# Kernel tuning notes

Measured on AMD Instinct MI355X. Metric: run time of the kernel, lower is better.

The kernel has to match this reference:

```python
import jax, jax.numpy as jnp
import numpy as np

K = 2
NOISE_STD = 1.0

def setup_inputs() -> dict:
    key = jax.random.key(0)
    k1, k2, k3 = jax.random.split(key, 3)
    N, D, E = 131072, 1024, 64
    x = jax.random.normal(k1, (N, D), dtype=jnp.float32)
    W = jax.random.normal(k2, (E, D), dtype=jnp.float32) * (1.0 / np.sqrt(D))
    b = jnp.zeros((E,), dtype=jnp.float32)
    noise = jax.random.normal(k3, (N, E), dtype=jnp.float32)
    return {"x": x, "W": W, "b": b, "noise": noise}

def reference(x, W, b, noise) -> jnp.ndarray:
    # clean logits: [N, E]
    clean_logits = jnp.einsum('nd,ed->ne', x, W) + b
    noisy_logits = clean_logits + noise * NOISE_STD
    topk_vals, topk_idx = jax.lax.top_k(noisy_logits, K)  # [N, K]
    topk_softmax = jax.nn.softmax(topk_vals, axis=-1)     # [N, K]
    rows = jnp.arange(x.shape[0])[:, None]                 # [N, 1]
    gate_weights = jnp.zeros_like(clean_logits).at[rows, topk_idx].set(topk_softmax)
    return gate_weights
```

## Files before the change

kernel.cpp:

```cpp
#include <hip/hip_runtime.h>
#include <math.h>


#define NEXP   64
#define BLOCK  256
#define TILE_M 128
#define DFIX   1024
#define KCF    32
#define NCH    32
#define NBUF   3
#define XCHB   16384
#define WCHB   8192
#define TAU    1e-3f
#define CAP    4096
#define WS_W_OFF 32768

typedef __attribute__((ext_vector_type(8)))  short bf16x8;
typedef __attribute__((ext_vector_type(16))) float f32x16;

__device__ __forceinline__ bool beats(float v, int e, float vo, int eo) {
    return (v > vo) || (v == vo && e < eo);
}

__device__ __forceinline__ void split2(float f0, float f1, unsigned int& hi, unsigned int& lo) {
    unsigned int u0 = __float_as_uint(f0), u1 = __float_as_uint(f1);
    unsigned int h0 = u0 & 0xFFFF0000u,  h1 = u1 & 0xFFFF0000u;
    float l0 = f0 - __uint_as_float(h0);
    float l1 = f1 - __uint_as_float(h1);
    hi = (u0 >> 16) | h1;
    lo = (__float_as_uint(l0) >> 16) | (__float_as_uint(l1) & 0xFFFF0000u);
}

__device__ __forceinline__ void gl_lds16(const void* g, void* l) {
    __builtin_amdgcn_global_load_lds((const __attribute__((address_space(1))) void*)g,
                                     (__attribute__((address_space(3))) void*)l,
                                     16, 0, 0);
}

__global__ void convW_kernel(const float* __restrict__ W, char* __restrict__ wsW) {
    const int e = blockIdx.x;
    const int t = threadIdx.x;
    const float* wp = W + e * DFIX + t * 8;
    float4 a  = *(const float4*)wp;
    float4 bq = *(const float4*)(wp + 4);
    unsigned int h[4], l[4];
    split2(a.x,  a.y,  h[0], l[0]);
    split2(a.z,  a.w,  h[1], l[1]);
    split2(bq.x, bq.y, h[2], l[2]);
    split2(bq.z, bq.w, h[3], l[3]);
    const int kk   = t >> 1;
    const int lh   = t & 1;
    const int lane = lh * 32 + (e & 31);
    const int g    = e >> 5;
    char* base = wsW + (size_t)(kk * 4 + g * 2) * 1024 + lane * 16;
    *(uint4*)(base)        = make_uint4(h[0], h[1], h[2], h[3]);
    *(uint4*)(base + 1024) = make_uint4(l[0], l[1], l[2], l[3]);
}

__global__ __launch_bounds__(BLOCK, 2)
void gate_mfma(const float* __restrict__ x, const float* __restrict__ bvec,
               const float* __restrict__ noise, const char* __restrict__ wsW,
               float* __restrict__ out, unsigned int* __restrict__ flags) {
    __shared__ __align__(16) char lds[NBUF * (XCHB + WCHB)];
    char* xls = lds;
    char* wls = lds + NBUF * XCHB;

    const int tid  = threadIdx.x;
    const int wv   = tid >> 6;
    const int lane = tid & 63;
    const int e0   = lane & 31;
    const int lh   = lane >> 5;
    const int blkRow0 = blockIdx.x * TILE_M;
    const int rowBase = blkRow0 + wv * 32;
    const int lr      = wv * 32 + e0;
    const int phase   = blockIdx.x & 31;

    f32x16 acc0 = (f32x16)0.0f;
    f32x16 acc1 = (f32x16)0.0f;

    auto STAGE = [&](int gc, int sl) {
        char* xb = xls + sl * XCHB;
        char* wb = wls + sl * WCHB;
        const size_t kbyte = (size_t)gc * (KCF * 4);
        #pragma unroll
        for (int j = 0; j < 4; j++) {
            const int s   = wv * 256 + j * 64 + lane;
            const int row = s >> 3;
            const int sp  = s & 7;
            const int seg = sp ^ (row & 7);
            const char* gp = (const char*)(x + (size_t)(blkRow0 + row) * DFIX)
                             + kbyte + seg * 16;
            gl_lds16(gp, xb + (size_t)(wv * 256 + j * 64) * 16);
        }
        #pragma unroll
        for (int i = 0; i < 2; i++) {
            const int fl = wv * 2 + i;
            const char* gp = wsW + (size_t)gc * WCHB + fl * 1024 + lane * 16;
            gl_lds16(gp, wb + fl * 1024);
        }
    };

    auto COMPUTE = [&](int sl) {
        const char* xb = xls + sl * XCHB;
        const char* wb = wls + sl * WCHB;
        #pragma unroll
        for (int ks = 0; ks < 2; ks++) {
            const int t0 = ks * 4 + lh * 2;
            const int4 xq0 = *(const int4*)(xb + lr * 128 + ((t0    ) ^ (lr & 7)) * 16);
            const int4 xq1 = *(const int4*)(xb + lr * 128 + ((t0 + 1) ^ (lr & 7)) * 16);
            const float4 xa = *(const float4*)&xq0;
            const float4 xc = *(const float4*)&xq1;
            union { bf16x8 v; unsigned int u[4]; } ah, al;
            split2(xa.x, xa.y, ah.u[0], al.u[0]);
            split2(xa.z, xa.w, ah.u[1], al.u[1]);
            split2(xc.x, xc.y, ah.u[2], al.u[2]);
            split2(xc.z, xc.w, ah.u[3], al.u[3]);
            union { bf16x8 v; int4 q; } b0h, b0l, b1h, b1l;
            b0h.q = *(const int4*)(wb + (ks * 4 + 0) * 1024 + lane * 16);
            b0l.q = *(const int4*)(wb + (ks * 4 + 1) * 1024 + lane * 16);
            b1h.q = *(const int4*)(wb + (ks * 4 + 2) * 1024 + lane * 16);
            b1l.q = *(const int4*)(wb + (ks * 4 + 3) * 1024 + lane * 16);
            acc0 = __builtin_amdgcn_mfma_f32_32x32x16_bf16(ah.v, b0h.v, acc0, 0, 0, 0);
            acc1 = __builtin_amdgcn_mfma_f32_32x32x16_bf16(ah.v, b1h.v, acc1, 0, 0, 0);
            acc0 = __builtin_amdgcn_mfma_f32_32x32x16_bf16(ah.v, b0l.v, acc0, 0, 0, 0);
            acc1 = __builtin_amdgcn_mfma_f32_32x32x16_bf16(ah.v, b1l.v, acc1, 0, 0, 0);
            acc0 = __builtin_amdgcn_mfma_f32_32x32x16_bf16(al.v, b0h.v, acc0, 0, 0, 0);
            acc1 = __builtin_amdgcn_mfma_f32_32x32x16_bf16(al.v, b1h.v, acc1, 0, 0, 0);
        }
    };

    STAGE(phase, 0);
    int slc = 0;
    #pragma unroll 1
    for (int c = 0; c < NCH - 1; c++) {
        const int sln = (slc + 1 == NBUF) ? 0 : slc + 1;
        STAGE((c + 1 + phase) & (NCH - 1), sln);
        asm volatile("s_waitcnt vmcnt(6)" ::: "memory");
        __builtin_amdgcn_s_barrier();
        __builtin_amdgcn_sched_barrier(0);
        COMPUTE(slc);
        slc = sln;
    }
    asm volatile("s_waitcnt vmcnt(0)" ::: "memory");
    __builtin_amdgcn_s_barrier();
    __builtin_amdgcn_sched_barrier(0);
    COMPUTE(slc);

    const float bb0 = bvec[e0], bb1 = bvec[e0 + 32];
    #pragma unroll
    for (int q = 0; q < 4; q++) {
        #pragma unroll
        for (int j = 0; j < 4; j++) {
            const int reg = q * 4 + j;
            const int r = rowBase + j + 8 * q + 4 * lh;
            const float n0 = noise[(size_t)r * NEXP + e0];
            const float n1 = noise[(size_t)r * NEXP + e0 + 32];
            const float v0 = (acc0[reg] + bb0) + n0;
            const float v1 = (acc1[reg] + bb1) + n1;

            float v1m, v2m, v3m = -1e30f; int e1m, e2m;
            if (beats(v0, e0, v1, e0 + 32)) { v1m = v0; e1m = e0;      v2m = v1; e2m = e0 + 32; }
            else                            { v1m = v1; e1m = e0 + 32; v2m = v0; e2m = e0;      }
            #pragma unroll
            for (int d = 1; d < 32; d <<= 1) {
                float ov1 = __shfl_xor(v1m, d); int oe1 = __shfl_xor(e1m, d);
                float ov2 = __shfl_xor(v2m, d); int oe2 = __shfl_xor(e2m, d);
                float ov3 = __shfl_xor(v3m, d);
                bool  aw  = beats(v1m, e1m, ov1, oe1);
                float a1v = aw ? v1m : ov1; int a1e = aw ? e1m : oe1;
                float b1v = aw ? ov1 : v1m; int b1e = aw ? oe1 : e1m;
                float a2v = aw ? v2m : ov2; int a2e = aw ? e2m : oe2;
                float b2v = aw ? ov2 : v2m;
                float a3v = aw ? v3m : ov3;
                bool  s2  = beats(a2v, a2e, b1v, b1e);
                v1m = a1v; e1m = a1e;
                v2m = s2 ? a2v : b1v; e2m = s2 ? a2e : b1e;
                v3m = s2 ? fmaxf(a3v, b1v) : fmaxf(a2v, b2v);
            }
            const float t   = __expf(v2m - v1m);
            const float inv = 1.0f / (1.0f + t);
            const float w1  = inv, w2 = t * inv;

            if (e0 == 0 && (v2m - v3m) < TAU) {
                unsigned int idx = atomicAdd(flags, 1u);
                if (idx < CAP) flags[1 + idx] = (unsigned int)r;
            }
            const int c0 = 2 * e0, c1 = c0 + 1;
            const float o0 = (c0 == e1m) ? w1 : (c0 == e2m) ? w2 : 0.0f;
            const float o1 = (c1 == e1m) ? w1 : (c1 == e2m) ? w2 : 0.0f;
            *(float2*)(out + (size_t)r * NEXP + c0) = make_float2(o0, o1);
        }
    }
}

__global__ void gate_repair(const float* __restrict__ x, const float* __restrict__ W,
                            const float* __restrict__ b, const float* __restrict__ noise,
                            float* __restrict__ out, const unsigned int* __restrict__ flags,
                            int D) {
    unsigned int cnt = flags[0];
    if (cnt > CAP) cnt = CAP;
    if (blockIdx.x >= cnt) return;
    const int r = (int)flags[1 + blockIdx.x];
    const int e = threadIdx.x;

    const float* xr = x + (size_t)r * D;
    const float* wr = W + (size_t)e * D;
    double s = 0.0;
    for (int d0 = 0; d0 < D; d0 += 4) {
        float4 xv = *(const float4*)(xr + d0);
        float4 wv = *(const float4*)(wr + d0);
        s += (double)xv.x * (double)wv.x;
        s += (double)xv.y * (double)wv.y;
        s += (double)xv.z * (double)wv.z;
        s += (double)xv.w * (double)wv.w;
    }
    const float clean = (float)s + b[e];
    const float v     = clean + noise[(size_t)r * NEXP + e];

    float v1 = v, v2 = -1e30f; int e1 = e, e2 = 99;
    for (int d = 1; d < 64; d <<= 1) {
        float ov1 = __shfl_xor(v1, d); int oe1 = __shfl_xor(e1, d);
        float ov2 = __shfl_xor(v2, d); int oe2 = __shfl_xor(e2, d);
        bool  aw  = beats(v1, e1, ov1, oe1);
        float a1v = aw ? v1 : ov1; int a1e = aw ? e1 : oe1;
        float b1v = aw ? ov1 : v1; int b1e = aw ? oe1 : e1;
        float a2v = aw ? v2 : ov2; int a2e = aw ? e2 : oe2;
        bool  s2  = beats(a2v, a2e, b1v, b1e);
        v1 = a1v; e1 = a1e;
        v2 = s2 ? a2v : b1v; e2 = s2 ? a2e : b1e;
    }
    const float t   = __expf(v2 - v1);
    const float inv = 1.0f / (1.0f + t);
    out[(size_t)r * NEXP + e] = (e == e1) ? inv : (e == e2) ? t * inv : 0.0f;
}

extern "C" void kernel_launch(void* const* d_in, const int* in_sizes, int n_in,
                              void* d_out, int out_size, void* d_ws, size_t ws_size,
                              hipStream_t stream) {
    const float* x     = (const float*)d_in[0];
    const float* W     = (const float*)d_in[1];
    const float* b     = (const float*)d_in[2];
    const float* noise = (const float*)d_in[3];
    float* out = (float*)d_out;

    const int E = in_sizes[2];
    const int D = in_sizes[1] / E;
    const int N = in_sizes[0] / D;

    unsigned int* flags = (unsigned int*)d_ws;
    char* wsW = (char*)d_ws + WS_W_OFF;

    convW_kernel<<<dim3(E), dim3(128), 0, stream>>>(W, wsW);
    hipMemsetAsync(d_ws, 0, sizeof(unsigned int), stream);
    gate_mfma<<<dim3(N / TILE_M), dim3(BLOCK), 0, stream>>>(x, b, noise, wsW, out, flags);
    gate_repair<<<dim3(CAP), dim3(64), 0, stream>>>(x, W, b, noise, out, flags, D);
}
```

Before: 218.2 us.

## Retile gate GEMM to 64-row tiles with W in registers and LDS top-k

Tiles shrink from 128 to 64 rows, and the four waves now split the work as 2 row groups by 2 expert groups. Each wave prefetches its W fragments straight from global memory into registers instead of staging W through LDS. The x chunks grow to 128 floats and are double-buffered, so there are fewer K iterations but an extra barrier per chunk. The epilogue writes the logits to swizzled LDS and then does a per-row top-k with 4 threads per row, a shorter shuffle reduction and float4 output stores. The cost is doubled W global traffic relative to rows and heavy register use for the 16 prefetched int4 fragments.

```diff
diff --git a/kernel.cpp b/kernel.cpp
--- a/kernel.cpp
+++ b/kernel.cpp
@@ -4,13 +4,11 @@
 
 #define NEXP   64
 #define BLOCK  256
-#define TILE_M 128
+#define TILE_M 64
 #define DFIX   1024
-#define KCF    32
-#define NCH    32
-#define NBUF   3
-#define XCHB   16384
-#define WCHB   8192
+#define KCF    128
+#define NCH    8
+#define XCHB   32768
 #define TAU    1e-3f
 #define CAP    4096
 #define WS_W_OFF 32768
@@ -61,53 +59,51 @@
 void gate_mfma(const float* __restrict__ x, const float* __restrict__ bvec,
                const float* __restrict__ noise, const char* __restrict__ wsW,
                float* __restrict__ out, unsigned int* __restrict__ flags) {
-    __shared__ __align__(16) char lds[NBUF * (XCHB + WCHB)];
-    char* xls = lds;
-    char* wls = lds + NBUF * XCHB;
+    __shared__ __align__(16) char lds[2 * XCHB];
 
     const int tid  = threadIdx.x;
     const int wv   = tid >> 6;
     const int lane = tid & 63;
     const int e0   = lane & 31;
     const int lh   = lane >> 5;
+    const int rg   = wv & 1;
+    const int cg   = wv >> 1;
     const int blkRow0 = blockIdx.x * TILE_M;
-    const int rowBase = blkRow0 + wv * 32;
-    const int lr      = wv * 32 + e0;
-    const int phase   = blockIdx.x & 31;
-
-    f32x16 acc0 = (f32x16)0.0f;
-    f32x16 acc1 = (f32x16)0.0f;
-
-    auto STAGE = [&](int gc, int sl) {
-        char* xb = xls + sl * XCHB;
-        char* wb = wls + sl * WCHB;
-        const size_t kbyte = (size_t)gc * (KCF * 4);
-        #pragma unroll
-        for (int j = 0; j < 4; j++) {
-            const int s   = wv * 256 + j * 64 + lane;
-            const int row = s >> 3;
-            const int sp  = s & 7;
-            const int seg = sp ^ (row & 7);
+    const int rowL  = rg * 32 + e0;
+    const int phase = blockIdx.x & (NCH - 1);
+
+    f32x16 acc = (f32x16)0.0f;
+
+    auto STAGE = [&](int gc, int buf) {
+        char* xb = lds + buf * XCHB;
+        #pragma unroll
+        for (int j = 0; j < 8; j++) {
+            const int s   = j * 256 + wv * 64 + lane;
+            const int row = s >> 5;
+            const int seg = (s & 31) ^ (row & 31);
             const char* gp = (const char*)(x + (size_t)(blkRow0 + row) * DFIX)
-                             + kbyte + seg * 16;
-            gl_lds16(gp, xb + (size_t)(wv * 256 + j * 64) * 16);
-        }
-        #pragma unroll
-        for (int i = 0; i < 2; i++) {
-            const int fl = wv * 2 + i;
-            const char* gp = wsW + (size_t)gc * WCHB + fl * 1024 + lane * 16;
-            gl_lds16(gp, wb + fl * 1024);
+                             + (size_t)gc * 512 + seg * 16;
+            gl_lds16(gp, xb + (size_t)(j * 256 + wv * 64) * 16);
         }
     };
 
-    auto COMPUTE = [&](int sl) {
-        const char* xb = xls + sl * XCHB;
-        const char* wb = wls + sl * WCHB;
-        #pragma unroll
-        for (int ks = 0; ks < 2; ks++) {
-            const int t0 = ks * 4 + lh * 2;
-            const int4 xq0 = *(const int4*)(xb + lr * 128 + ((t0    ) ^ (lr & 7)) * 16);
-            const int4 xq1 = *(const int4*)(xb + lr * 128 + ((t0 + 1) ^ (lr & 7)) * 16);
+    int4 wreg[16];
+    auto WPRE = [&](int gc) {
+        const char* base = wsW + (size_t)(gc * 32 + cg * 2) * 1024 + lane * 16;
+        #pragma unroll
+        for (int ks = 0; ks < 8; ks++) {
+            wreg[ks * 2 + 0] = *(const int4*)(base + (ks * 4 + 0) * 1024);
+            wreg[ks * 2 + 1] = *(const int4*)(base + (ks * 4 + 1) * 1024);
+        }
+    };
+
+    auto COMPUTE = [&](int buf) {
+        const char* xb = lds + buf * XCHB;
+        #pragma unroll
+        for (int ks = 0; ks < 8; ks++) {
+            const int g0 = ks * 4 + lh * 2;
+            const int4 xq0 = *(const int4*)(xb + rowL * 512 + ((g0    ) ^ (rowL & 31)) * 16);
+            const int4 xq1 = *(const int4*)(xb + rowL * 512 + ((g0 + 1) ^ (rowL & 31)) * 16);
             const float4 xa = *(const float4*)&xq0;
             const float4 xc = *(const float4*)&xq1;
             union { bf16x8 v; unsigned int u[4]; } ah, al;
@@ -115,80 +111,101 @@
             split2(xa.z, xa.w, ah.u[1], al.u[1]);
             split2(xc.x, xc.y, ah.u[2], al.u[2]);
             split2(xc.z, xc.w, ah.u[3], al.u[3]);
-            union { bf16x8 v; int4 q; } b0h, b0l, b1h, b1l;
-            b0h.q = *(const int4*)(wb + (ks * 4 + 0) * 1024 + lane * 16);
-            b0l.q = *(const int4*)(wb + (ks * 4 + 1) * 1024 + lane * 16);
-            b1h.q = *(const int4*)(wb + (ks * 4 + 2) * 1024 + lane * 16);
-            b1l.q = *(const int4*)(wb + (ks * 4 + 3) * 1024 + lane * 16);
-            acc0 = __builtin_amdgcn_mfma_f32_32x32x16_bf16(ah.v, b0h.v, acc0, 0, 0, 0);
-            acc1 = __builtin_amdgcn_mfma_f32_32x32x16_bf16(ah.v, b1h.v, acc1, 0, 0, 0);
-            acc0 = __builtin_amdgcn_mfma_f32_32x32x16_bf16(ah.v, b0l.v, acc0, 0, 0, 0);
-            acc1 = __builtin_amdgcn_mfma_f32_32x32x16_bf16(ah.v, b1l.v, acc1, 0, 0, 0);
-            acc0 = __builtin_amdgcn_mfma_f32_32x32x16_bf16(al.v, b0h.v, acc0, 0, 0, 0);
-            acc1 = __builtin_amdgcn_mfma_f32_32x32x16_bf16(al.v, b1h.v, acc1, 0, 0, 0);
+            union { bf16x8 v; int4 q; } bh, bl;
+            bh.q = wreg[ks * 2 + 0];
+            bl.q = wreg[ks * 2 + 1];
+            acc = __builtin_amdgcn_mfma_f32_32x32x16_bf16(ah.v, bh.v, acc, 0, 0, 0);
+            acc = __builtin_amdgcn_mfma_f32_32x32x16_bf16(ah.v, bl.v, acc, 0, 0, 0);
+            acc = __builtin_amdgcn_mfma_f32_32x32x16_bf16(al.v, bh.v, acc, 0, 0, 0);
         }
     };
 
     STAGE(phase, 0);
-    int slc = 0;
     #pragma unroll 1
     for (int c = 0; c < NCH - 1; c++) {
-        const int sln = (slc + 1 == NBUF) ? 0 : slc + 1;
-        STAGE((c + 1 + phase) & (NCH - 1), sln);
-        asm volatile("s_waitcnt vmcnt(6)" ::: "memory");
+        WPRE((c + phase) & (NCH - 1));
+        STAGE((c + 1 + phase) & (NCH - 1), (c + 1) & 1);
+        asm volatile("s_waitcnt vmcnt(8)" ::: "memory");
         __builtin_amdgcn_s_barrier();
         __builtin_amdgcn_sched_barrier(0);
-        COMPUTE(slc);
-        slc = sln;
-    }
+        COMPUTE(c & 1);
+        __builtin_amdgcn_s_barrier();
+    }
+    WPRE((NCH - 1 + phase) & (NCH - 1));
     asm volatile("s_waitcnt vmcnt(0)" ::: "memory");
     __builtin_amdgcn_s_barrier();
     __builtin_amdgcn_sched_barrier(0);
-    COMPUTE(slc);
-
-    const float bb0 = bvec[e0], bb1 = bvec[e0 + 32];
+    COMPUTE((NCH - 1) & 1);
+
+    const float bb = bvec[cg * 32 + e0];
     #pragma unroll
     for (int q = 0; q < 4; q++) {
         #pragma unroll
         for (int j = 0; j < 4; j++) {
             const int reg = q * 4 + j;
-            const int r = rowBase + j + 8 * q + 4 * lh;
-            const float n0 = noise[(size_t)r * NEXP + e0];
-            const float n1 = noise[(size_t)r * NEXP + e0 + 32];
-            const float v0 = (acc0[reg] + bb0) + n0;
-            const float v1 = (acc1[reg] + bb1) + n1;
-
-            float v1m, v2m, v3m = -1e30f; int e1m, e2m;
-            if (beats(v0, e0, v1, e0 + 32)) { v1m = v0; e1m = e0;      v2m = v1; e2m = e0 + 32; }
-            else                            { v1m = v1; e1m = e0 + 32; v2m = v0; e2m = e0;      }
+            const int rl  = rg * 32 + j + 8 * q + 4 * lh;
+            const int r   = blkRow0 + rl;
+            const int col = cg * 32 + e0;
+            const float v = (acc[reg] + bb) + noise[(size_t)r * NEXP + col];
+            const int slot = (col >> 2) ^ (rl & 15);
+            *(float*)(lds + rl * 256 + slot * 16 + (col & 3) * 4) = v;
+        }
+    }
+    __syncthreads();
+
+    {
+        const int trow = tid >> 2;
+        const int qd   = tid & 3;
+        float v1 = -1e30f, v2 = -1e30f, v3 = -1e30f;
+        int   e1 = 99, e2 = 99;
+        #pragma unroll
+        for (int i = 0; i < 4; i++) {
+            const int slot = (qd * 4 + i) ^ (trow & 15);
+            const float4 f = *(const float4*)(lds + trow * 256 + slot * 16);
             #pragma unroll
-            for (int d = 1; d < 32; d <<= 1) {
-                float ov1 = __shfl_xor(v1m, d); int oe1 = __shfl_xor(e1m, d);
-                float ov2 = __shfl_xor(v2m, d); int oe2 = __shfl_xor(e2m, d);
-                float ov3 = __shfl_xor(v3m, d);
-                bool  aw  = beats(v1m, e1m, ov1, oe1);
-                float a1v = aw ? v1m : ov1; int a1e = aw ? e1m : oe1;
-                float b1v = aw ? ov1 : v1m; int b1e = aw ? oe1 : e1m;
-                float a2v = aw ? v2m : ov2; int a2e = aw ? e2m : oe2;
-                float b2v = aw ? ov2 : v2m;
-                float a3v = aw ? v3m : ov3;
-                bool  s2  = beats(a2v, a2e, b1v, b1e);
-                v1m = a1v; e1m = a1e;
-                v2m = s2 ? a2v : b1v; e2m = s2 ? a2e : b1e;
-                v3m = s2 ? fmaxf(a3v, b1v) : fmaxf(a2v, b2v);
+            for (int m = 0; m < 4; m++) {
+                const float v = (m == 0) ? f.x : (m == 1) ? f.y : (m == 2) ? f.z : f.w;
+                const int   e = qd * 16 + i * 4 + m;
+                if (beats(v, e, v1, e1))      { v3 = v2; v2 = v1; e2 = e1; v1 = v; e1 = e; }
+                else if (beats(v, e, v2, e2)) { v3 = v2; v2 = v;  e2 = e; }
+                else                          { v3 = fmaxf(v3, v); }
             }
-            const float t   = __expf(v2m - v1m);
-            const float inv = 1.0f / (1.0f + t);
-            const float w1  = inv, w2 = t * inv;
-
-            if (e0 == 0 && (v2m - v3m) < TAU) {
-                unsigned int idx = atomicAdd(flags, 1u);
-                if (idx < CAP) flags[1 + idx] = (unsigned int)r;
+        }
+        #pragma unroll
+        for (int d = 1; d < 4; d <<= 1) {
+            float ov1 = __shfl_xor(v1, d); int oe1 = __shfl_xor(e1, d);
+            float ov2 = __shfl_xor(v2, d); int oe2 = __shfl_xor(e2, d);
+            float ov3 = __shfl_xor(v3, d);
+            bool  aw  = beats(v1, e1, ov1, oe1);
+            float a1v = aw ? v1 : ov1; int a1e = aw ? e1 : oe1;
+            float b1v = aw ? ov1 : v1; int b1e = aw ? oe1 : e1;
+            float a2v = aw ? v2 : ov2; int a2e = aw ? e2 : oe2;
+            float b2v = aw ? ov2 : v2;
+            float a3v = aw ? v3 : ov3;
+            bool  s2  = beats(a2v, a2e, b1v, b1e);
+            v1 = a1v; e1 = a1e;
+            v2 = s2 ? a2v : b1v; e2 = s2 ? a2e : b1e;
+            v3 = s2 ? fmaxf(a3v, b1v) : fmaxf(a2v, b2v);
+        }
+        const float t   = __expf(v2 - v1);
+        const float inv = 1.0f / (1.0f + t);
+        const float w1  = inv, w2 = t * inv;
+        const int   r   = blkRow0 + trow;
+
+        if (qd == 0 && (v2 - v3) < TAU) {
+            unsigned int idx = atomicAdd(flags, 1u);
+            if (idx < CAP) flags[1 + idx] = (unsigned int)r;
+        }
+        float* op = out + (size_t)r * NEXP + qd * 16;
+        #pragma unroll
+        for (int i = 0; i < 4; i++) {
+            float o[4];
+            #pragma unroll
+            for (int m = 0; m < 4; m++) {
+                const int e = qd * 16 + i * 4 + m;
+                o[m] = (e == e1) ? w1 : (e == e2) ? w2 : 0.0f;
             }
-            const int c0 = 2 * e0, c1 = c0 + 1;
-            const float o0 = (c0 == e1m) ? w1 : (c0 == e2m) ? w2 : 0.0f;
-            const float o1 = (c1 == e1m) ? w1 : (c1 == e2m) ? w2 : 0.0f;
-            *(float2*)(out + (size_t)r * NEXP + c0) = make_float2(o0, o1);
+            *(float4*)(op + i * 4) = make_float4(o[0], o[1], o[2], o[3]);
         }
     }
 }
```

Measured after the change: 204.8 us. -6.2%, faster.
